# Kernel tuning notes

Hardware: AMD Instinct MI355X
Metric: run time of the kernel (lower is better)

The kernel has to match this reference:

```python
import jax, jax.numpy as jnp
import numpy as np

N = 512
L = 1.0
DX = L / (N - 1)
DT = 1e-07
NUM_STEPS = 200
MB = 256  # material_boundary[1]


def setup_inputs() -> dict:
    key = jax.random.key(0)
    u0 = jax.random.normal(key, (N, N), dtype=jnp.float32)
    one = jnp.ones((1,), dtype=jnp.float32)
    return {"u0": u0, "k1": one, "k2": one, "alpha1": one, "alpha2": one}


def reference(u0, k1, k2, alpha1, alpha2):
    k1 = k1.reshape(())
    k2 = k2.reshape(())
    alpha1 = alpha1.reshape(())
    alpha2 = alpha2.reshape(())
    col_is_left = (jnp.arange(N) < MB)  # columns [:MB] get material 1
    material_map = jnp.broadcast_to(jnp.where(col_is_left, alpha1, alpha2), (N, N))
    k_map = jnp.broadcast_to(jnp.where(col_is_left, k1, k2), (N, N))
    alpha = material_map[1:-1, 1:-1]
    kappa = k_map[1:-1, 1:-1]
    dx2 = DX * DX
    ii = MB - 1  # interface column index
    k_left = k_map[:, ii]
    k_right = k_map[:, ii + 1]

    def step(T, _):
        Tc = T[1:-1, 1:-1]
        T_xx = (T[:-2, 1:-1] - 2.0 * Tc + T[2:, 1:-1]) / dx2
        T_yy = (T[1:-1, :-2] - 2.0 * Tc + T[1:-1, 2:]) / dx2
        T_x = (T[2:, 1:-1] - T[:-2, 1:-1]) / (2.0 * DX)
        T_y = (T[1:-1, 2:] - T[1:-1, :-2]) / (2.0 * DX)
        Tn_int = (Tc
                  - DT * (Tc ** 2 * T_x - Tc * T_y) * kappa
                  + DT * alpha * (T_xx + T_yy)
                  + DT * kappa * (Tc ** 3 - Tc ** 2 + Tc))
        Tn = T.at[1:-1, 1:-1].set(Tn_int)
        # material interface condition (uses old T values, as in source)
        Tn = Tn.at[:, ii].set((k_left * T[:, ii + 1] + k_right * T[:, ii - 1]) / (k_left + k_right))
        # Neumann-like boundary copies, in the same order as the source
        Tn = Tn.at[0, :].set(Tn[1, :])
        Tn = Tn.at[-1, :].set(Tn[-2, :])
        Tn = Tn.at[:, 0].set(Tn[:, 1])
        Tn = Tn.at[:, -1].set(Tn[:, -2])
        return Tn, Tn

    # torch code records T before each of num_steps iterations and returns [1:],
    # i.e. the states after steps 1..num_steps-1
    _, ys = jax.lax.scan(step, u0, None, length=NUM_STEPS - 1)
    return ys  # (NUM_STEPS-1, N, N)
```

## Files before the change

kernel.cpp:

```cpp
#include <hip/hip_runtime.h>

#define GN 512
#define GNN (GN * GN)
#define NSTEPS 199

#define TS 16
#define KS 8
#define PR 4
#define PC 4

__constant__ const float kCdiff = (float)(1e-7 * 511.0 * 511.0);
__constant__ const float kCadv  = (float)(1e-7 * 511.0 / 2.0);
__constant__ const float kCrea  = 1e-7f;

#define DPP_SHR1(x) __int_as_float(__builtin_amdgcn_mov_dpp( \
    __float_as_int(x), 0x138, 0xf, 0xf, true))
#define DPP_SHL1(x) __int_as_float(__builtin_amdgcn_mov_dpp( \
    __float_as_int(x), 0x130, 0xf, 0xf, true))
#define BPERM(a, x) __int_as_float(__builtin_amdgcn_ds_bpermute( \
    (a), __float_as_int(x)))

#define DO_STEP(SRC, DST, TMI, TPI, TMO, TPO, SIDX)                           \
{                                                                             \
    float tlE[PR], trE[PR];                                                   \
    _Pragma("unroll") for (int r = 0; r < PR; ++r) {                          \
        tlE[r] = DPP_SHR1(SRC[r][PC - 1]);                                    \
        trE[r] = DPP_SHL1(SRC[r][0]);                                         \
    }                                                                         \
    _Pragma("unroll") for (int ri = 0; ri < PR; ++ri) {                       \
        const int r = (ri == 0) ? 1 : (ri == 1) ? 2 : (ri == 2) ? 0 : 3;      \
        _Pragma("unroll") for (int c = 0; c < PC; ++c) {                      \
            const float tc = SRC[r][c];                                       \
            const float tm = (r > 0)      ? SRC[r - 1][c] : TMI[c];           \
            const float tp = (r < PR - 1) ? SRC[r + 1][c] : TPI[c];           \
            const float tl = (c > 0)      ? SRC[r][c - 1] : tlE[r];           \
            const float tr = (c < PC - 1) ? SRC[r][c + 1] : trE[r];           \
            const float t2 = tc * tc;                                         \
            const float dv = tp - tm;                                         \
            const float dh = tr - tl;                                         \
            const float lap = __builtin_fmaf(-4.0f, tc, (tm + tp) + (tl + tr)); \
            const float advt = __builtin_fmaf(t2, dv, -(tc * dh));            \
            const float reat = __builtin_fmaf(t2, tc - 1.0f, tc);             \
            float v = __builtin_fmaf(nckA[c], advt, tc);                      \
            v = __builtin_fmaf(ckD[c], lap, v);                               \
            v = __builtin_fmaf(ckR[c], reat, v);                              \
            if (hasIface) {                                                   \
                const float vif = __builtin_fmaf(k1, tr, k2 * tl) * inv12;    \
                v = (pc0 + c == 255) ? vif : v;                               \
            }                                                                 \
            DST[r][c] = v;                                                    \
        }                                                                     \
    }                                                                         \
             \
    if (fTop && rg == 2) { _Pragma("unroll")                                  \
        for (int c = 0; c < PC; ++c) DST[0][c] = DST[1][c]; }                 \
    if (fBot && rg == 5) { _Pragma("unroll")                                  \
        for (int c = 0; c < PC; ++c) DST[PR - 1][c] = DST[PR - 2][c]; }       \
    if (fL && cg == 2) { _Pragma("unroll")                                    \
        for (int r = 0; r < PR; ++r) DST[r][0] = DST[r][1]; }                 \
    if (fR && cg == 5) { _Pragma("unroll")                                    \
        for (int r = 0; r < PR; ++r) DST[r][PC - 1] = DST[r][PC - 2]; }       \
             \
    _Pragma("unroll") for (int c = 0; c < PC; ++c) {                          \
        TMO[c] = BPERM(aU, DST[PR - 1][c]);                                   \
        TPO[c] = BPERM(aD, DST[0][c]);                                        \
    }                                                                         \
    if (storeLane) {                                                          \
        float* __restrict__ dsts = dstbase + (size_t)(SIDX) * GNN + lofs;     \
        _Pragma("unroll") for (int r = 0; r < PR; ++r) {                      \
            float4 v4;                                                        \
            v4.x = DST[r][0]; v4.y = DST[r][1];                               \
            v4.z = DST[r][2]; v4.w = DST[r][3];                               \
            *reinterpret_cast<float4*>(dsts + r * GN) = v4;                   \
        }                                                                     \
    }                                                                         \
}

__global__ __launch_bounds__(64) void adr_fused(
    const float* __restrict__ src, float* __restrict__ dstbase, int nsteps,
    const float* __restrict__ pk1, const float* __restrict__ pk2,
    const float* __restrict__ pa1, const float* __restrict__ pa2)
{
    const int lane = threadIdx.x & 63;
    const int cg = lane & 7;
    const int rg = lane >> 3;
    const int bx = blockIdx.x & 31;
    const int by = blockIdx.x >> 5;
    const int rb = by * TS - KS;
    const int cb = bx * TS - KS;
    const int pr0 = rb + rg * PR;
    const int pc0 = cb + cg * PC;
    const int lofs = pr0 * GN + pc0;

    const float k1 = pk1[0];
    const float k2 = pk2[0];
    const float a1 = pa1[0];
    const float a2 = pa2[0];
    const float inv12 = 1.0f / (k1 + k2);

    float nckA[PC], ckD[PC], ckR[PC];
    #pragma unroll
    for (int c = 0; c < PC; ++c) {
        const int gc = pc0 + c;
        const float kap = (gc < 256) ? k1 : k2;
        const float alp = (gc < 256) ? a1 : a2;
        nckA[c] = -(kap * kCadv);
        ckD[c]  = alp * kCdiff;
        ckR[c]  = kCrea * kap;
    }

    const int aU = ((lane + 56) & 63) << 2;
    const int aD = ((lane + 8) & 63) << 2;

    const bool interior = (bx > 0 && bx < 31 && by > 0 && by < 31);
    const bool hasIface = (bx == 15 || bx == 16);
    const bool fTop = (by == 0), fBot = (by == 31);
    const bool fL = (bx == 0), fR = (bx == 31);
    const bool storeLane = (rg >= 2 && rg <= 5 && cg >= 2 && cg <= 5);

    float A[PR][PC], B[PR][PC];
    if (interior) {
        #pragma unroll
        for (int r = 0; r < PR; ++r) {
            const float4 v = *reinterpret_cast<const float4*>(
                src + (pr0 + r) * GN + pc0);
            A[r][0] = v.x; A[r][1] = v.y; A[r][2] = v.z; A[r][3] = v.w;
        }
    } else {
        #pragma unroll
        for (int r = 0; r < PR; ++r) {
            const int gr = min(max(pr0 + r, 0), GN - 1);
            #pragma unroll
            for (int c = 0; c < PC; ++c) {
                const int gc = min(max(pc0 + c, 0), GN - 1);
                A[r][c] = src[gr * GN + gc];
            }
        }
    }

    float tm0[PC], tp0[PC], tm1[PC], tp1[PC];
    #pragma unroll
    for (int c = 0; c < PC; ++c) {
        tm0[c] = BPERM(aU, A[PR - 1][c]);
        tp0[c] = BPERM(aD, A[0][c]);
    }

    #pragma unroll
    for (int s = 0; s < KS; s += 2) {
        if (s >= nsteps) break;
        DO_STEP(A, B, tm0, tp0, tm1, tp1, s)
        if (s + 1 >= nsteps) break;
        DO_STEP(B, A, tm1, tp1, tm0, tp0, s + 1)
    }
}

extern "C" void kernel_launch(void* const* d_in, const int* in_sizes, int n_in,
                              void* d_out, int out_size, void* d_ws, size_t ws_size,
                              hipStream_t stream) {
    (void)in_sizes; (void)n_in; (void)out_size; (void)d_ws; (void)ws_size;

    const float* u0 = (const float*)d_in[0];
    const float* k1 = (const float*)d_in[1];
    const float* k2 = (const float*)d_in[2];
    const float* a1 = (const float*)d_in[3];
    const float* a2 = (const float*)d_in[4];
    float* out = (float*)d_out;

    const dim3 block(64);
    const dim3 grid((GN / TS) * (GN / TS));

    const float* src = u0;
    int step = 0;
    while (step < NSTEPS) {
        const int ns = (NSTEPS - step < KS) ? (NSTEPS - step) : KS;
        float* dstbase = out + (size_t)step * GNN;
        adr_fused<<<grid, block, 0, stream>>>(src, dstbase, ns, k1, k2, a1, a2);
        src = dstbase + (size_t)(ns - 1) * GNN;
        step += ns;
    }
}
```

Measured before the change: 371.1 us.

## Replace per-block kernel launches with persistent cooperative kernel and neighbor flags

Instead of launching one kernel per group of 8 time steps (25 launches), a single cooperative persistent kernel loops over the step blocks. Each tile publishes a completion flag after storing its last step, and waits only on its 3x3 neighbor tiles' flags before reloading the halo from global memory. This removes repeated launch and grid-wide barrier overhead. In exchange it adds spin-wait polling, scalar agent-scope atomic loads and stores in place of vectorized float4 accesses, and a hipMemsetAsync of the flag buffer on every call.

```diff
diff --git a/kernel.cpp b/kernel.cpp
--- a/kernel.cpp
+++ b/kernel.cpp
@@ -6,6 +6,7 @@
 
 #define TS 16
 #define KS 8
+#define NKB ((NSTEPS + KS - 1) / KS)
 #define PR 4
 #define PC 4
 
@@ -20,7 +21,17 @@
 #define BPERM(a, x) __int_as_float(__builtin_amdgcn_ds_bpermute( \
     (a), __float_as_int(x)))
 
-#define DO_STEP(SRC, DST, TMI, TPI, TMO, TPO, SIDX)                           \
+__device__ __forceinline__ float agent_load_f(const float* p) {
+    unsigned u = __hip_atomic_load((const unsigned*)p, __ATOMIC_RELAXED,
+                                   __HIP_MEMORY_SCOPE_AGENT);
+    return __uint_as_float(u);
+}
+__device__ __forceinline__ void agent_store_f(float* p, float v) {
+    __hip_atomic_store((unsigned*)p, __float_as_uint(v), __ATOMIC_RELAXED,
+                       __HIP_MEMORY_SCOPE_AGENT);
+}
+
+#define DO_STEP(SRC, DST, TMI, TPI, TMO, TPO, SIDX, FINAL)                    \
 {                                                                             \
     float tlE[PR], trE[PR];                                                   \
     _Pragma("unroll") for (int r = 0; r < PR; ++r) {                          \
@@ -66,26 +77,34 @@
         TPO[c] = BPERM(aD, DST[0][c]);                                        \
     }                                                                         \
     if (storeLane) {                                                          \
-        float* __restrict__ dsts = dstbase + (size_t)(SIDX) * GNN + lofs;     \
-        _Pragma("unroll") for (int r = 0; r < PR; ++r) {                      \
-            float4 v4;                                                        \
-            v4.x = DST[r][0]; v4.y = DST[r][1];                               \
-            v4.z = DST[r][2]; v4.w = DST[r][3];                               \
-            *reinterpret_cast<float4*>(dsts + r * GN) = v4;                   \
+        float* __restrict__ dsts = out + (size_t)(SIDX) * GNN + lofs;         \
+        if (FINAL) {                                                          \
+            _Pragma("unroll") for (int r = 0; r < PR; ++r)                    \
+                _Pragma("unroll") for (int c = 0; c < PC; ++c)                \
+                    agent_store_f(dsts + r * GN + c, DST[r][c]);              \
+        } else {                                                              \
+            _Pragma("unroll") for (int r = 0; r < PR; ++r) {                  \
+                float4 v4;                                                    \
+                v4.x = DST[r][0]; v4.y = DST[r][1];                           \
+                v4.z = DST[r][2]; v4.w = DST[r][3];                           \
+                *reinterpret_cast<float4*>(dsts + r * GN) = v4;               \
+            }                                                                 \
         }                                                                     \
     }                                                                         \
 }
 
-__global__ __launch_bounds__(64) void adr_fused(
-    const float* __restrict__ src, float* __restrict__ dstbase, int nsteps,
+__global__ __launch_bounds__(64) void adr_persist(
+    const float* __restrict__ u0, float* __restrict__ out,
     const float* __restrict__ pk1, const float* __restrict__ pk2,
-    const float* __restrict__ pa1, const float* __restrict__ pa2)
+    const float* __restrict__ pa1, const float* __restrict__ pa2,
+    unsigned* __restrict__ flags)
 {
     const int lane = threadIdx.x & 63;
     const int cg = lane & 7;
     const int rg = lane >> 3;
     const int bx = blockIdx.x & 31;
     const int by = blockIdx.x >> 5;
+    const int tileId = blockIdx.x;
     const int rb = by * TS - KS;
     const int cb = bx * TS - KS;
     const int pr0 = rb + rg * PR;
@@ -118,46 +137,90 @@
     const bool fL = (bx == 0), fR = (bx == 31);
     const bool storeLane = (rg >= 2 && rg <= 5 && cg >= 2 && cg <= 5);
 
+    int rowoff[PR], coloff[PC];
+    #pragma unroll
+    for (int r = 0; r < PR; ++r)
+        rowoff[r] = min(max(pr0 + r, 0), GN - 1) * GN;
+    #pragma unroll
+    for (int c = 0; c < PC; ++c)
+        coloff[c] = min(max(pc0 + c, 0), GN - 1);
+
+    int nbid = 0;
+    {
+        const int q = lane + (lane >= 4 ? 1 : 0);
+        const int nbx = min(max(bx + (q % 3) - 1, 0), 31);
+        const int nby = min(max(by + (q / 3) - 1, 0), 31);
+        nbid = nby * 32 + nbx;
+    }
+
     float A[PR][PC], B[PR][PC];
-    if (interior) {
+    float tm0[PC], tp0[PC], tm1[PC], tp1[PC];
+
+    #pragma unroll 1
+    for (int kb = 0; kb < NKB; ++kb) {
+        const int ns = (NSTEPS - kb * KS < KS) ? (NSTEPS - kb * KS) : KS;
+
+        if (kb == 0) {
+            if (interior) {
+                #pragma unroll
+                for (int r = 0; r < PR; ++r) {
+                    const float4 v = *reinterpret_cast<const float4*>(
+                        u0 + (pr0 + r) * GN + pc0);
+                    A[r][0] = v.x; A[r][1] = v.y;
+                    A[r][2] = v.z; A[r][3] = v.w;
+                }
+            } else {
+                #pragma unroll
+                for (int r = 0; r < PR; ++r)
+                    #pragma unroll
+                    for (int c = 0; c < PC; ++c)
+                        A[r][c] = u0[rowoff[r] + coloff[c]];
+            }
+        } else {
+            bool ready = false;
+            while (!ready) {
+                unsigned v = 0xFFFFFFFFu;
+                if (lane < 8)
+                    v = __hip_atomic_load(&flags[nbid], __ATOMIC_RELAXED,
+                                          __HIP_MEMORY_SCOPE_AGENT);
+                ready = __all((lane >= 8) || (v >= (unsigned)kb));
+                if (!ready) __builtin_amdgcn_s_sleep(4);
+            }
+            asm volatile("" ::: "memory");
+            const float* sl = out + (size_t)(kb * KS - 1) * GNN;
+            #pragma unroll
+            for (int r = 0; r < PR; ++r)
+                #pragma unroll
+                for (int c = 0; c < PC; ++c)
+                    A[r][c] = agent_load_f(sl + rowoff[r] + coloff[c]);
+        }
+
         #pragma unroll
-        for (int r = 0; r < PR; ++r) {
-            const float4 v = *reinterpret_cast<const float4*>(
-                src + (pr0 + r) * GN + pc0);
-            A[r][0] = v.x; A[r][1] = v.y; A[r][2] = v.z; A[r][3] = v.w;
+        for (int c = 0; c < PC; ++c) {
+            tm0[c] = BPERM(aU, A[PR - 1][c]);
+            tp0[c] = BPERM(aD, A[0][c]);
         }
-    } else {
+
+        const int base = kb * KS;
         #pragma unroll
-        for (int r = 0; r < PR; ++r) {
-            const int gr = min(max(pr0 + r, 0), GN - 1);
-            #pragma unroll
-            for (int c = 0; c < PC; ++c) {
-                const int gc = min(max(pc0 + c, 0), GN - 1);
-                A[r][c] = src[gr * GN + gc];
-            }
+        for (int s = 0; s < KS; s += 2) {
+            if (s >= ns) break;
+            DO_STEP(A, B, tm0, tp0, tm1, tp1, base + s, (s == ns - 1))
+            if (s + 1 >= ns) break;
+            DO_STEP(B, A, tm1, tp1, tm0, tp0, base + s + 1, (s + 1 == ns - 1))
         }
-    }
-
-    float tm0[PC], tp0[PC], tm1[PC], tp1[PC];
-    #pragma unroll
-    for (int c = 0; c < PC; ++c) {
-        tm0[c] = BPERM(aU, A[PR - 1][c]);
-        tp0[c] = BPERM(aD, A[0][c]);
-    }
-
-    #pragma unroll
-    for (int s = 0; s < KS; s += 2) {
-        if (s >= nsteps) break;
-        DO_STEP(A, B, tm0, tp0, tm1, tp1, s)
-        if (s + 1 >= nsteps) break;
-        DO_STEP(B, A, tm1, tp1, tm0, tp0, s + 1)
+
+        asm volatile("s_waitcnt vmcnt(0)" ::: "memory");
+        if (lane == 0)
+            __hip_atomic_store(&flags[tileId], (unsigned)(kb + 1),
+                               __ATOMIC_RELAXED, __HIP_MEMORY_SCOPE_AGENT);
     }
 }
 
 extern "C" void kernel_launch(void* const* d_in, const int* in_sizes, int n_in,
                               void* d_out, int out_size, void* d_ws, size_t ws_size,
                               hipStream_t stream) {
-    (void)in_sizes; (void)n_in; (void)out_size; (void)d_ws; (void)ws_size;
+    (void)in_sizes; (void)n_in; (void)out_size; (void)ws_size;
 
     const float* u0 = (const float*)d_in[0];
     const float* k1 = (const float*)d_in[1];
@@ -165,17 +228,14 @@
     const float* a1 = (const float*)d_in[3];
     const float* a2 = (const float*)d_in[4];
     float* out = (float*)d_out;
-
-    const dim3 block(64);
-    const dim3 grid((GN / TS) * (GN / TS));
-
-    const float* src = u0;
-    int step = 0;
-    while (step < NSTEPS) {
-        const int ns = (NSTEPS - step < KS) ? (NSTEPS - step) : KS;
-        float* dstbase = out + (size_t)step * GNN;
-        adr_fused<<<grid, block, 0, stream>>>(src, dstbase, ns, k1, k2, a1, a2);
-        src = dstbase + (size_t)(ns - 1) * GNN;
-        step += ns;
-    }
-}
+    unsigned* flags = (unsigned*)d_ws;
+
+    const int ntiles = (GN / TS) * (GN / TS);
+
+    hipMemsetAsync(flags, 0, ntiles * sizeof(unsigned), stream);
+
+    void* args[] = {(void*)&u0, (void*)&out, (void*)&k1, (void*)&k2,
+                    (void*)&a1, (void*)&a2, (void*)&flags};
+    hipLaunchCooperativeKernel((void*)adr_persist, dim3(ntiles), dim3(64),
+                               args, 0, stream);
+}
```

New measurement: 440.9 us. 18.8% more time.
